# Optimization experiments

Measured on AMD Instinct MI355X. Metric: run time of the kernel, lower is better.

The kernel has to match this reference:

```python
import jax, jax.numpy as jnp
import numpy as np

TIME_LEN = 8
JOINT_NUM = 22
SEQ = TIME_LEN * JOINT_NUM  # 176
H_NUM = 8
H_DIM = 64
NEG = -9e15


def build_t_mask():
    # ones everywhere, zero the 22x22 diagonal (same-frame) blocks, then add identity
    t = np.ones((SEQ, SEQ), dtype=np.float32)
    for i in range(TIME_LEN):
        b = i * JOINT_NUM
        t[b:b + JOINT_NUM, b:b + JOINT_NUM] = 0.0
    t += np.eye(SEQ, dtype=np.float32)
    return jnp.asarray(t)


def setup_inputs() -> dict:
    key = jax.random.key(0)
    ks = jax.random.split(key, 7)
    B, S, D_IN = 512, SEQ, 128
    D_MODEL = H_NUM * H_DIM
    s = 1.0 / np.sqrt(D_IN)
    return {
        "x": jax.random.normal(ks[0], (B, S, D_IN), dtype=jnp.float32),
        "Wq": jax.random.normal(ks[1], (D_IN, D_MODEL), dtype=jnp.float32) * s,
        "bq": jax.random.normal(ks[2], (D_MODEL,), dtype=jnp.float32) * 0.01,
        "Wk": jax.random.normal(ks[3], (D_IN, D_MODEL), dtype=jnp.float32) * s,
        "bk": jax.random.normal(ks[4], (D_MODEL,), dtype=jnp.float32) * 0.01,
        "Wv": jax.random.normal(ks[5], (D_IN, D_MODEL), dtype=jnp.float32) * s,
        "bv": jax.random.normal(ks[6], (D_MODEL,), dtype=jnp.float32) * 0.01,
    }


def reference(x, Wq, bq, Wk, bk, Wv, bv):
    B = x.shape[0]
    mask = build_t_mask()  # [S, S], values in {0, 1}
    # projections; dropout is inference-mode identity; value path has ReLU
    q = (x @ Wq + bq).reshape(B, -1, H_NUM, H_DIM).transpose(0, 2, 1, 3)  # [B,H,S,D]
    k = (x @ Wk + bk).reshape(B, -1, H_NUM, H_DIM).transpose(0, 2, 1, 3)
    v = jax.nn.relu(x @ Wv + bv).reshape(B, -1, H_NUM, H_DIM).transpose(0, 2, 1, 3)
    scores = jnp.einsum("bhqd,bhkd->bhqk", q, k) / jnp.sqrt(jnp.float32(H_DIM))
    # temporal domain: multiplicative mask + large-negative additive fill
    scores = scores * mask + (1.0 - mask) * NEG
    p = jax.nn.softmax(scores, axis=-1)
    out = jnp.einsum("bhqk,bhkd->bhqd", p, v)
    return out.transpose(0, 2, 1, 3).reshape(B, -1, H_NUM * H_DIM)
```

## Files before the change

kernel.cpp:

```cpp
#include <hip/hip_runtime.h>
#include <hip/hip_bf16.h>

#define JOINTS   22
#define SEQ      176
#define DIN      128
#define NHEAD    8
#define HD       64
#define DMODEL   512
#define NMT      11

typedef __bf16 bf16x8 __attribute__((ext_vector_type(8)));
typedef float  f32x4  __attribute__((ext_vector_type(4)));

__device__ __forceinline__ unsigned short f2bf(float f) {
  __hip_bfloat16 h = __float2bfloat16(f);
  return __builtin_bit_cast(unsigned short, h);
}
__device__ __forceinline__ float bf2f(unsigned short u) {
  __hip_bfloat16 h = __builtin_bit_cast(__hip_bfloat16, u);
  return __bfloat162float(h);
}

#define WT_E    0u
#define BIAS_E  196608u
#define Q_E     198144u
#define PERQKV  46137344u
#define K_E     (Q_E + PERQKV)
#define V_E     (K_E + PERQKV)
#define WS_NEED ((size_t)(V_E + PERQKV) * 2)

__global__ __launch_bounds__(256) void prep_kernel(
    const float* __restrict__ Wq, const float* __restrict__ bq,
    const float* __restrict__ Wk, const float* __restrict__ bk,
    const float* __restrict__ Wv, const float* __restrict__ bv,
    unsigned short* __restrict__ ws)
{
  int idx = blockIdx.x * 256 + threadIdx.x;
  int which = idx >> 16;
  int rem = idx & 65535;
  int n = rem >> 7, k = rem & 127;
  const float* W = (which == 0) ? Wq : (which == 1 ? Wk : Wv);
  float scale = (which == 0) ? 0.125f : 1.0f;
  ws[WT_E + idx] = f2bf(W[k * DMODEL + n] * scale);
  if (idx < 1536) {
    int w2 = idx >> 9, n2 = idx & 511;
    const float* bb = (w2 == 0) ? bq : (w2 == 1 ? bk : bv);
    float s2 = (w2 == 0) ? 0.125f : 1.0f;
    ws[BIAS_E + idx] = f2bf(bb[n2] * s2);
  }
}

__global__ __launch_bounds__(256) void qkv_gemm_kernel(
    const float* __restrict__ x, unsigned short* __restrict__ ws)
{
  __shared__ unsigned short Xs[128 * 136];
  __shared__ unsigned short Wt[128 * 136];
  const int tid  = threadIdx.x;
  const int lane = tid & 63, wave = tid >> 6;
  const int l15  = lane & 15, quad = lane >> 4;
  const int m0 = blockIdx.x * 128;
  const int nb = blockIdx.y;
  const int wm = (wave >> 1) * 64, wn = (wave & 1) * 64;

  {
    const float4* x4 = reinterpret_cast<const float4*>(x + (size_t)m0 * DIN);
    #pragma unroll
    for (int i = 0; i < 16; ++i) {
      int c = tid + i * 256;
      int row = c >> 5, col4 = c & 31;
      float4 v = x4[c];
      uint2 pk;
      pk.x = (unsigned)f2bf(v.x) | ((unsigned)f2bf(v.y) << 16);
      pk.y = (unsigned)f2bf(v.z) | ((unsigned)f2bf(v.w) << 16);
      *reinterpret_cast<uint2*>(&Xs[row * 136 + col4 * 4]) = pk;
    }
  }

  int gb[4], gs[4];
  int vb[4], vs[4];
  #pragma unroll
  for (int mt = 0; mt < 4; ++mt) {
    int g = m0 + wm + mt * 16 + l15;
    gb[mt] = g / 176; gs[mt] = g - gb[mt] * 176;
    int g0 = m0 + wm + mt * 16 + quad * 4;
    vb[mt] = g0 / 176; vs[mt] = g0 - vb[mt] * 176;
  }

  for (int which = 0; which < 3; ++which) {
    __syncthreads();
    {
      const uint4* wsrc = reinterpret_cast<const uint4*>(
          ws + WT_E + which * 65536 + nb * 128 * 128);
      #pragma unroll
      for (int i = 0; i < 8; ++i) {
        int c = tid + i * 256;
        int row = c >> 4, col8 = c & 15;
        *reinterpret_cast<uint4*>(&Wt[row * 136 + col8 * 8]) = wsrc[c];
      }
    }
    __syncthreads();

    f32x4 acc[16];
    #pragma unroll
    for (int i = 0; i < 16; ++i) acc[i] = (f32x4){0.f, 0.f, 0.f, 0.f};

    #pragma unroll
    for (int kk = 0; kk < 4; ++kk) {
      bf16x8 a[4], bfr[4];
      #pragma unroll
      for (int mt = 0; mt < 4; ++mt)
        a[mt] = *reinterpret_cast<const bf16x8*>(
            &Xs[(wm + mt * 16 + l15) * 136 + kk * 32 + quad * 8]);
      #pragma unroll
      for (int nt = 0; nt < 4; ++nt)
        bfr[nt] = *reinterpret_cast<const bf16x8*>(
            &Wt[(wn + nt * 16 + l15) * 136 + kk * 32 + quad * 8]);
      if (which != 2) {
        #pragma unroll
        for (int mt = 0; mt < 4; ++mt)
          #pragma unroll
          for (int nt = 0; nt < 4; ++nt)
            acc[mt * 4 + nt] = __builtin_amdgcn_mfma_f32_16x16x32_bf16(
                bfr[nt], a[mt], acc[mt * 4 + nt], 0, 0, 0);
      } else {
        #pragma unroll
        for (int mt = 0; mt < 4; ++mt)
          #pragma unroll
          for (int nt = 0; nt < 4; ++nt)
            acc[mt * 4 + nt] = __builtin_amdgcn_mfma_f32_16x16x32_bf16(
                a[mt], bfr[nt], acc[mt * 4 + nt], 0, 0, 0);
      }
    }

    if (which != 2) {
      unsigned short* dst = ws + ((which == 0) ? Q_E : K_E);
      #pragma unroll
      for (int nt = 0; nt < 4; ++nt) {
        int c0 = nb * 128 + wn + nt * 16 + quad * 4;
        int h = c0 >> 6, d0 = c0 & 63;
        uint2 bpk = *reinterpret_cast<const uint2*>(
            ws + BIAS_E + which * 512 + c0);
        float b0 = bf2f((unsigned short)(bpk.x & 0xffffu));
        float b1 = bf2f((unsigned short)(bpk.x >> 16));
        float b2 = bf2f((unsigned short)(bpk.y & 0xffffu));
        float b3 = bf2f((unsigned short)(bpk.y >> 16));
        #pragma unroll
        for (int mt = 0; mt < 4; ++mt) {
          f32x4 ac = acc[mt * 4 + nt];
          uint2 pk;
          pk.x = (unsigned)f2bf(ac[0] + b0) | ((unsigned)f2bf(ac[1] + b1) << 16);
          pk.y = (unsigned)f2bf(ac[2] + b2) | ((unsigned)f2bf(ac[3] + b3) << 16);
          *reinterpret_cast<uint2*>(
              &dst[((size_t)(gb[mt] * 8 + h) * 176 + gs[mt]) * 64 + d0]) = pk;
        }
      }
    } else {
      unsigned short* dst = ws + V_E;
      #pragma unroll
      for (int nt = 0; nt < 4; ++nt) {
        int c = nb * 128 + wn + nt * 16 + l15;
        int h = c >> 6, d = c & 63;
        float bs = bf2f(ws[BIAS_E + 1024 + c]);
        #pragma unroll
        for (int mt = 0; mt < 4; ++mt) {
          f32x4 ac = acc[mt * 4 + nt];
          float v0 = fmaxf(ac[0] + bs, 0.f), v1 = fmaxf(ac[1] + bs, 0.f);
          float v2 = fmaxf(ac[2] + bs, 0.f), v3 = fmaxf(ac[3] + bs, 0.f);
          uint2 pk;
          pk.x = (unsigned)f2bf(v0) | ((unsigned)f2bf(v1) << 16);
          pk.y = (unsigned)f2bf(v2) | ((unsigned)f2bf(v3) << 16);
          *reinterpret_cast<uint2*>(
              &dst[((size_t)(vb[mt] * 8 + h) * 64 + d) * 176 + vs[mt]]) = pk;
        }
      }
    }
  }
}

#define KLD 72
#define VLD 184
#define PLD 184

__global__ __launch_bounds__(256) void attn_kernel(
    const unsigned short* __restrict__ ws, float* __restrict__ out)
{
  __shared__ unsigned short Ks[SEQ * KLD];
  __shared__ unsigned short Vt[HD * VLD];
  __shared__ unsigned short Ps[4][16 * PLD];

  const int tid  = threadIdx.x;
  const int lane = tid & 63, wave = tid >> 6;
  const int l15  = lane & 15, quad = lane >> 4;
  const int bh = blockIdx.x;
  const int b = bh >> 3, h = bh & 7;

  const unsigned short* qp = ws + Q_E + (size_t)bh * 11264;
  const unsigned short* kp = ws + K_E + (size_t)bh * 11264;
  const unsigned short* vp = ws + V_E + (size_t)bh * 11264;

  const uint4 z4 = {0u, 0u, 0u, 0u};
  const bf16x8 zfrag = __builtin_bit_cast(bf16x8, z4);

  bf16x8 aq[3][2];
  #pragma unroll
  for (int i = 0; i < 3; ++i) {
    int mt = wave + 4 * i;
    aq[i][0] = *reinterpret_cast<const bf16x8*>(qp + (mt * 16 + l15) * 64 + quad * 8);
    aq[i][1] = *reinterpret_cast<const bf16x8*>(qp + (mt * 16 + l15) * 64 + 32 + quad * 8);
  }

  {
    const uint4* ks4 = reinterpret_cast<const uint4*>(kp);
    #pragma unroll
    for (int i = 0; i < 6; ++i) {
      int c = tid + i * 256;
      if (c < 1408) {
        int row = c >> 3, col = c & 7;
        *reinterpret_cast<uint4*>(&Ks[row * KLD + col * 8]) = ks4[c];
      }
    }
  }
  {
    const uint4* vs4 = reinterpret_cast<const uint4*>(vp);
    #pragma unroll
    for (int i = 0; i < 6; ++i) {
      int c = tid + i * 256;
      if (c < 1408) {
        int row = c / 22, col = c - row * 22;
        *reinterpret_cast<uint4*>(&Vt[row * VLD + col * 8]) = vs4[c];
      }
    }
  }
  __syncthreads();

  unsigned short* Pw = Ps[wave];

  #pragma unroll
  for (int i = 0; i < 3; ++i) {
    const int mt = wave + 4 * i;

    f32x4 sc[NMT];
    #pragma unroll
    for (int nt = 0; nt < NMT; ++nt) {
      bf16x8 k0 = *reinterpret_cast<const bf16x8*>(
          &Ks[(nt * 16 + l15) * KLD + quad * 8]);
      bf16x8 k1 = *reinterpret_cast<const bf16x8*>(
          &Ks[(nt * 16 + l15) * KLD + 32 + quad * 8]);
      f32x4 acc = {0.f, 0.f, 0.f, 0.f};
      acc = __builtin_amdgcn_mfma_f32_16x16x32_bf16(k0, aq[i][0], acc, 0, 0, 0);
      acc = __builtin_amdgcn_mfma_f32_16x16x32_bf16(k1, aq[i][1], acc, 0, 0, 0);
      sc[nt] = acc;
    }

    const int q  = mt * 16 + l15;
    const int lo = (q / JOINTS) * JOINTS;
    const int hi = lo + JOINTS;

    float mx0 = -3.0e38f, mx1 = -3.0e38f, mx2 = -3.0e38f, mx3 = -3.0e38f;
    #pragma unroll
    for (int nt = 0; nt < NMT; ++nt) {
      #pragma unroll
      for (int r = 0; r < 4; ++r) {
        int k = nt * 16 + quad * 4 + r;
        bool msk = (k >= lo) && (k < hi) && (k != q);
        float v = msk ? -1.0e30f : sc[nt][r];
        sc[nt][r] = v;
        if (r == 0) mx0 = fmaxf(mx0, v);
        else if (r == 1) mx1 = fmaxf(mx1, v);
        else if (r == 2) mx2 = fmaxf(mx2, v);
        else mx3 = fmaxf(mx3, v);
      }
    }
    float mx = fmaxf(fmaxf(mx0, mx1), fmaxf(mx2, mx3));
    mx = fmaxf(mx, __shfl_xor(mx, 16));
    mx = fmaxf(mx, __shfl_xor(mx, 32));

    float s0 = 0.f, s1 = 0.f, s2 = 0.f, s3 = 0.f;
    #pragma unroll
    for (int nt = 0; nt < NMT; ++nt) {
      float e0 = __expf(sc[nt][0] - mx);
      float e1 = __expf(sc[nt][1] - mx);
      float e2 = __expf(sc[nt][2] - mx);
      float e3 = __expf(sc[nt][3] - mx);
      sc[nt][0] = e0; sc[nt][1] = e1; sc[nt][2] = e2; sc[nt][3] = e3;
      s0 += e0; s1 += e1; s2 += e2; s3 += e3;
    }
    float sum = (s0 + s1) + (s2 + s3);
    sum += __shfl_xor(sum, 16);
    sum += __shfl_xor(sum, 32);
    float rinv = 1.0f / sum;

    #pragma unroll
    for (int nt = 0; nt < NMT; ++nt) {
      float p0 = sc[nt][0] * rinv, p1 = sc[nt][1] * rinv;
      float p2 = sc[nt][2] * rinv, p3 = sc[nt][3] * rinv;
      uint2 pk;
      pk.x = (unsigned)f2bf(p0) | ((unsigned)f2bf(p1) << 16);
      pk.y = (unsigned)f2bf(p2) | ((unsigned)f2bf(p3) << 16);
      *reinterpret_cast<uint2*>(&Pw[l15 * PLD + nt * 16 + quad * 4]) = pk;
    }

    bf16x8 ap[6];
    #pragma unroll
    for (int kk = 0; kk < 6; ++kk) {
      bool act = (kk < 5) || (quad < 2);
      int off = act ? (kk * 32 + quad * 8) : 0;
      bf16x8 v = *reinterpret_cast<const bf16x8*>(&Pw[l15 * PLD + off]);
      ap[kk] = act ? v : zfrag;
    }

    #pragma unroll
    for (int nt_o = 0; nt_o < 4; ++nt_o) {
      f32x4 acc = {0.f, 0.f, 0.f, 0.f};
      #pragma unroll
      for (int kk = 0; kk < 6; ++kk) {
        bool act = (kk < 5) || (quad < 2);
        int off = act ? (kk * 32 + quad * 8) : 0;
        bf16x8 bv = *reinterpret_cast<const bf16x8*>(
            &Vt[(nt_o * 16 + l15) * VLD + off]);
        acc = __builtin_amdgcn_mfma_f32_16x16x32_bf16(ap[kk], bv, acc, 0, 0, 0);
      }
      if (mt < NMT) {
        #pragma unroll
        for (int r = 0; r < 4; ++r) {
          int qq = mt * 16 + quad * 4 + r;
          out[((size_t)b * SEQ + qq) * DMODEL + h * HD + nt_o * 16 + l15] =
              acc[r];
        }
      }
    }
  }
}

#define BLK      704
#define XS_LD 136
#define WS_LD 136
#define QK_LD 72
#define PV_LD 184

struct __align__(16) SMem {
  union {
    struct {
      unsigned short Xs[SEQ * XS_LD];
      unsigned short Ws[HD  * WS_LD];
    } p1;
    unsigned short Ps[SEQ * PV_LD];
  } u;
  unsigned short Qs[SEQ * QK_LD];
  unsigned short Ks[SEQ * QK_LD];
  unsigned short Vt[HD  * PV_LD];
};

__global__ __launch_bounds__(BLK) void mha_fused_kernel(
    const float* __restrict__ x,
    const float* __restrict__ Wq, const float* __restrict__ bq,
    const float* __restrict__ Wk, const float* __restrict__ bk,
    const float* __restrict__ Wv, const float* __restrict__ bv,
    float* __restrict__ out)
{
  __shared__ SMem sm;
  const int tid  = threadIdx.x;
  const int lane = tid & 63;
  const int wave = tid >> 6;
  const int l15  = lane & 15;
  const int quad = lane >> 4;
  const int b    = blockIdx.x >> 3;
  const int h    = blockIdx.x & 7;

  const uint4 z4 = {0u, 0u, 0u, 0u};
  const bf16x8 zfrag = __builtin_bit_cast(bf16x8, z4);

  {
    const float4* xg = reinterpret_cast<const float4*>(x + (size_t)b * (SEQ * DIN));
    #pragma unroll
    for (int i = 0; i < 8; ++i) {
      int c = tid + i * BLK;
      int row  = c >> 5;
      int col4 = c & 31;
      float4 v = xg[c];
      uint2 pk;
      pk.x = (unsigned)f2bf(v.x) | ((unsigned)f2bf(v.y) << 16);
      pk.y = (unsigned)f2bf(v.z) | ((unsigned)f2bf(v.w) << 16);
      *reinterpret_cast<uint2*>(&sm.u.p1.Xs[row * XS_LD + col4 * 4]) = pk;
    }
  }

  const float* Wptr[3] = {Wq, Wk, Wv};
  const float* Bptr[3] = {bq, bk, bv};

  for (int m = 0; m < 3; ++m) {
    for (int k = wave; k < DIN; k += NMT)
      sm.u.p1.Ws[lane * WS_LD + k] = f2bf(Wptr[m][(size_t)k * DMODEL + h * HD + lane]);
    __syncthreads();

    const int mt = wave;
    bf16x8 a[4];
    #pragma unroll
    for (int kk = 0; kk < 4; ++kk)
      a[kk] = *reinterpret_cast<const bf16x8*>(
          &sm.u.p1.Xs[(mt * 16 + l15) * XS_LD + kk * 32 + quad * 8]);

    #pragma unroll
    for (int nt = 0; nt < 4; ++nt) {
      f32x4 acc = {0.f, 0.f, 0.f, 0.f};
      #pragma unroll
      for (int kk = 0; kk < 4; ++kk) {
        bf16x8 bb = *reinterpret_cast<const bf16x8*>(
            &sm.u.p1.Ws[(nt * 16 + l15) * WS_LD + kk * 32 + quad * 8]);
        acc = __builtin_amdgcn_mfma_f32_16x16x32_bf16(a[kk], bb, acc, 0, 0, 0);
      }
      float bs = Bptr[m][h * HD + nt * 16 + l15];
      if (m == 0) {
        #pragma unroll
        for (int r = 0; r < 4; ++r)
          sm.Qs[(mt * 16 + quad * 4 + r) * QK_LD + nt * 16 + l15] =
              f2bf((acc[r] + bs) * 0.125f);
      } else if (m == 1) {
        #pragma unroll
        for (int r = 0; r < 4; ++r)
          sm.Ks[(mt * 16 + quad * 4 + r) * QK_LD + nt * 16 + l15] =
              f2bf(acc[r] + bs);
      } else {
        float v0 = fmaxf(acc[0] + bs, 0.f), v1 = fmaxf(acc[1] + bs, 0.f);
        float v2 = fmaxf(acc[2] + bs, 0.f), v3 = fmaxf(acc[3] + bs, 0.f);
        uint2 pk;
        pk.x = (unsigned)f2bf(v0) | ((unsigned)f2bf(v1) << 16);
        pk.y = (unsigned)f2bf(v2) | ((unsigned)f2bf(v3) << 16);
        *reinterpret_cast<uint2*>(
            &sm.Vt[(nt * 16 + l15) * PV_LD + mt * 16 + quad * 4]) = pk;
      }
    }
    __syncthreads();
  }

  {
    const int mt = wave;
    bf16x8 aq0 = *reinterpret_cast<const bf16x8*>(
        &sm.Qs[(mt * 16 + l15) * QK_LD + 0 + quad * 8]);
    bf16x8 aq1 = *reinterpret_cast<const bf16x8*>(
        &sm.Qs[(mt * 16 + l15) * QK_LD + 32 + quad * 8]);

    f32x4 sc[NMT];
    #pragma unroll
    for (int nt = 0; nt < NMT; ++nt) {
      f32x4 acc = {0.f, 0.f, 0.f, 0.f};
      bf16x8 k0 = *reinterpret_cast<const bf16x8*>(
          &sm.Ks[(nt * 16 + l15) * QK_LD + 0 + quad * 8]);
      bf16x8 k1 = *reinterpret_cast<const bf16x8*>(
          &sm.Ks[(nt * 16 + l15) * QK_LD + 32 + quad * 8]);
      acc = __builtin_amdgcn_mfma_f32_16x16x32_bf16(aq0, k0, acc, 0, 0, 0);
      acc = __builtin_amdgcn_mfma_f32_16x16x32_bf16(aq1, k1, acc, 0, 0, 0);
      sc[nt] = acc;
    }

    float rinv[4];
    #pragma unroll
    for (int r = 0; r < 4; ++r) {
      const int q  = mt * 16 + quad * 4 + r;
      const int fq = q / JOINTS;
      float mx = -3.0e38f;
      #pragma unroll
      for (int nt = 0; nt < NMT; ++nt) {
        int c = nt * 16 + l15;
        bool masked = ((c / JOINTS) == fq) && (c != q);
        float v = masked ? -1.0e30f : sc[nt][r];
        sc[nt][r] = v;
        mx = fmaxf(mx, v);
      }
      mx = fmaxf(mx, __shfl_xor(mx, 1));
      mx = fmaxf(mx, __shfl_xor(mx, 2));
      mx = fmaxf(mx, __shfl_xor(mx, 4));
      mx = fmaxf(mx, __shfl_xor(mx, 8));
      float sum = 0.f;
      #pragma unroll
      for (int nt = 0; nt < NMT; ++nt) {
        float e = __expf(sc[nt][r] - mx);
        sum += e;
        sm.u.Ps[q * PV_LD + nt * 16 + l15] = f2bf(e);
      }
      sum += __shfl_xor(sum, 1);
      sum += __shfl_xor(sum, 2);
      sum += __shfl_xor(sum, 4);
      sum += __shfl_xor(sum, 8);
      rinv[r] = 1.0f / sum;
    }

    #pragma unroll
    for (int nt = 0; nt < 4; ++nt) {
      f32x4 acc = {0.f, 0.f, 0.f, 0.f};
      #pragma unroll
      for (int kk = 0; kk < 6; ++kk) {
        bool act = (kk < 5) || (quad < 2);
        int off = act ? (kk * 32 + quad * 8) : 0;
        bf16x8 ap  = *reinterpret_cast<const bf16x8*>(
            &sm.u.Ps[(mt * 16 + l15) * PV_LD + off]);
        bf16x8 bv8 = *reinterpret_cast<const bf16x8*>(
            &sm.Vt[(nt * 16 + l15) * PV_LD + off]);
        if (!act) { ap = zfrag; bv8 = zfrag; }
        acc = __builtin_amdgcn_mfma_f32_16x16x32_bf16(ap, bv8, acc, 0, 0, 0);
      }
      #pragma unroll
      for (int r = 0; r < 4; ++r) {
        int q = mt * 16 + quad * 4 + r;
        out[((size_t)b * SEQ + q) * DMODEL + h * HD + nt * 16 + l15] =
            acc[r] * rinv[r];
      }
    }
  }
}

extern "C" void kernel_launch(void* const* d_in, const int* in_sizes, int n_in,
                              void* d_out, int out_size, void* d_ws, size_t ws_size,
                              hipStream_t stream) {
  const float* x  = (const float*)d_in[0];
  const float* Wq = (const float*)d_in[1];
  const float* bq = (const float*)d_in[2];
  const float* Wk = (const float*)d_in[3];
  const float* bk = (const float*)d_in[4];
  const float* Wv = (const float*)d_in[5];
  const float* bv = (const float*)d_in[6];
  const int B = in_sizes[0] / (SEQ * DIN);

  if (ws_size >= WS_NEED && B == 512) {
    unsigned short* ws = (unsigned short*)d_ws;
    hipLaunchKernelGGL(prep_kernel, dim3(768), dim3(256), 0, stream,
                       Wq, bq, Wk, bk, Wv, bv, ws);
    hipLaunchKernelGGL(qkv_gemm_kernel, dim3(704, 4), dim3(256), 0, stream,
                       x, ws);
    hipLaunchKernelGGL(attn_kernel, dim3(4096), dim3(256), 0, stream,
                       (const unsigned short*)ws, (float*)d_out);
  } else {
    hipLaunchKernelGGL(mha_fused_kernel, dim3(B * NHEAD), dim3(BLK), 0, stream,
                       x, Wq, bq, Wk, bk, Wv, bv, (float*)d_out);
  }
}
```

Baseline: 482.0 us.

## Feed softmax probabilities to PV MFMA directly from registers, dropping LDS round-trip

The softmax output is no longer staged through per-wave shared memory. Instead the score accumulator layout is reused directly as the A operand of the PV MFMA, with two 16-column score tiles packed into one 8-element fragment. The V reads are permuted to match that k ordering. This removes the P store/load through LDS and about 23KB of shared memory, and it adds launch_bounds occupancy 3. The cost is more, smaller 8-byte V loads from LDS.

Result: faster. 459.1 us (-4.7%).

```diff
diff --git a/kernel.cpp b/kernel.cpp
--- a/kernel.cpp
+++ b/kernel.cpp
@@ -179,14 +179,12 @@
 
 #define KLD 72
 #define VLD 184
-#define PLD 184
-
-__global__ __launch_bounds__(256) void attn_kernel(
+
+__global__ __launch_bounds__(256, 3) void attn_kernel(
     const unsigned short* __restrict__ ws, float* __restrict__ out)
 {
   __shared__ unsigned short Ks[SEQ * KLD];
   __shared__ unsigned short Vt[HD * VLD];
-  __shared__ unsigned short Ps[4][16 * PLD];
 
   const int tid  = threadIdx.x;
   const int lane = tid & 63, wave = tid >> 6;
@@ -197,9 +195,6 @@
   const unsigned short* qp = ws + Q_E + (size_t)bh * 11264;
   const unsigned short* kp = ws + K_E + (size_t)bh * 11264;
   const unsigned short* vp = ws + V_E + (size_t)bh * 11264;
-
-  const uint4 z4 = {0u, 0u, 0u, 0u};
-  const bf16x8 zfrag = __builtin_bit_cast(bf16x8, z4);
 
   bf16x8 aq[3][2];
   #pragma unroll
@@ -232,8 +227,6 @@
     }
   }
   __syncthreads();
-
-  unsigned short* Pw = Ps[wave];
 
   #pragma unroll
   for (int i = 0; i < 3; ++i) {
@@ -290,35 +283,42 @@
     sum += __shfl_xor(sum, 32);
     float rinv = 1.0f / sum;
 
-    #pragma unroll
-    for (int nt = 0; nt < NMT; ++nt) {
-      float p0 = sc[nt][0] * rinv, p1 = sc[nt][1] * rinv;
-      float p2 = sc[nt][2] * rinv, p3 = sc[nt][3] * rinv;
-      uint2 pk;
-      pk.x = (unsigned)f2bf(p0) | ((unsigned)f2bf(p1) << 16);
-      pk.y = (unsigned)f2bf(p2) | ((unsigned)f2bf(p3) << 16);
-      *reinterpret_cast<uint2*>(&Pw[l15 * PLD + nt * 16 + quad * 4]) = pk;
-    }
-
-    bf16x8 ap[6];
-    #pragma unroll
-    for (int kk = 0; kk < 6; ++kk) {
-      bool act = (kk < 5) || (quad < 2);
-      int off = act ? (kk * 32 + quad * 8) : 0;
-      bf16x8 v = *reinterpret_cast<const bf16x8*>(&Pw[l15 * PLD + off]);
-      ap[kk] = act ? v : zfrag;
+    bf16x8 af[6];
+    #pragma unroll
+    for (int pr = 0; pr < 6; ++pr) {
+      const int ntA = 2 * pr, ntB = 2 * pr + 1;
+      uint4 a4;
+      {
+        float p0 = sc[ntA][0] * rinv, p1 = sc[ntA][1] * rinv;
+        float p2 = sc[ntA][2] * rinv, p3 = sc[ntA][3] * rinv;
+        a4.x = (unsigned)f2bf(p0) | ((unsigned)f2bf(p1) << 16);
+        a4.y = (unsigned)f2bf(p2) | ((unsigned)f2bf(p3) << 16);
+      }
+      if (pr < 5) {
+        float p0 = sc[ntB][0] * rinv, p1 = sc[ntB][1] * rinv;
+        float p2 = sc[ntB][2] * rinv, p3 = sc[ntB][3] * rinv;
+        a4.z = (unsigned)f2bf(p0) | ((unsigned)f2bf(p1) << 16);
+        a4.w = (unsigned)f2bf(p2) | ((unsigned)f2bf(p3) << 16);
+      } else {
+        a4.z = 0u; a4.w = 0u;
+      }
+      af[pr] = __builtin_bit_cast(bf16x8, a4);
     }
 
     #pragma unroll
     for (int nt_o = 0; nt_o < 4; ++nt_o) {
+      const unsigned short* vrow = &Vt[(nt_o * 16 + l15) * VLD];
       f32x4 acc = {0.f, 0.f, 0.f, 0.f};
       #pragma unroll
-      for (int kk = 0; kk < 6; ++kk) {
-        bool act = (kk < 5) || (quad < 2);
-        int off = act ? (kk * 32 + quad * 8) : 0;
-        bf16x8 bv = *reinterpret_cast<const bf16x8*>(
-            &Vt[(nt_o * 16 + l15) * VLD + off]);
-        acc = __builtin_amdgcn_mfma_f32_16x16x32_bf16(ap[kk], bv, acc, 0, 0, 0);
+      for (int pr = 0; pr < 6; ++pr) {
+        const int ntA = 2 * pr, ntB = 2 * pr + 1;
+        uint2 blo = *reinterpret_cast<const uint2*>(vrow + ntA * 16 + quad * 4);
+        uint2 bhi = (pr < 5)
+            ? *reinterpret_cast<const uint2*>(vrow + ntB * 16 + quad * 4)
+            : (uint2){0u, 0u};
+        uint4 b4; b4.x = blo.x; b4.y = blo.y; b4.z = bhi.x; b4.w = bhi.y;
+        bf16x8 bf = __builtin_bit_cast(bf16x8, b4);
+        acc = __builtin_amdgcn_mfma_f32_16x16x32_bf16(af[pr], bf, acc, 0, 0, 0);
       }
       if (mt < NMT) {
         #pragma unroll
```
